# Kernel tuning notes

Measured on AMD Instinct MI355X. Metric: run time of the kernel, lower is better.

Reference implementation:

```python
import jax, jax.numpy as jnp
import numpy as np

LRELU = 0.2
EPS_LN = 1e-5
EPS_BN = 1e-5


def _seg_softmax(logits, seg, n):
    # softmax over edges grouped by destination node (PyG softmax), logits [E,H]
    m = jax.ops.segment_max(logits, seg, num_segments=n)
    e = jnp.exp(logits - m[seg])
    s = jax.ops.segment_sum(e, seg, num_segments=n)
    return e / (s[seg] + 1e-16)


def _gat(x, src, dst, n, W, a_src, a_dst, b, H, C):
    # PyG GATConv, concat=False (mean over heads), leaky_relu slope 0.2
    h = (x @ W).reshape(n, H, C)
    e = (h * a_src).sum(-1)[src] + (h * a_dst).sum(-1)[dst]  # [E,H]
    e = jnp.where(e > 0, e, LRELU * e)
    alpha = _seg_softmax(e, dst, n)
    out = jax.ops.segment_sum(h[src] * alpha[:, :, None], dst, num_segments=n)  # [N,H,C]
    return out.mean(1) + b


def _gcn(x, src, dst, n, W, b):
    # PyG GCNConv with symmetric normalization; edge list already contains self loops
    deg = jax.ops.segment_sum(jnp.ones(src.shape, x.dtype), dst, num_segments=n)
    dis = jnp.where(deg > 0, jax.lax.rsqrt(jnp.maximum(deg, 1e-12)), 0.0)
    h = x @ W
    w = (dis[src] * dis[dst])[:, None]
    return jax.ops.segment_sum(h[src] * w, dst, num_segments=n) + b


def _ln(x, g, b):
    mu = x.mean(-1, keepdims=True)
    v = x.var(-1, keepdims=True)
    return (x - mu) * jax.lax.rsqrt(v + EPS_LN) * g + b


def _bn_eval(x, g, b, rm, rv):
    return (x - rm) * jax.lax.rsqrt(rv + EPS_BN) * g + b


def _forward(x, edge_index, gin, bti, rmi, rvi, W1, as1, ad1, b1, Wg1, bg1,
             W2, as2, ad2, b2, Wg2, bg2, Ws, bs, Wf, bf,
             g1, be1, g2, be2, g3, be3, Wc1, bc1, gbn, bbn, rmb, rvb, Wc2, bc2):
    n = x.shape[0]
    xn = _bn_eval(x, gin, bti, rmi, rvi)
    sl = jnp.arange(n, dtype=edge_index.dtype)
    src = jnp.concatenate([edge_index[0], sl])
    dst = jnp.concatenate([edge_index[1], sl])
    # GAT1 (4 heads, 128) -> LN -> relu
    x1 = _gat(xn, src, dst, n, W1, as1, ad1, b1, 4, 128)
    x1 = jax.nn.relu(_ln(x1, g1, be1))
    # GCN1 -> relu
    x1g = jax.nn.relu(_gcn(x1, src, dst, n, Wg1, bg1))
    # GAT2 (2 heads, 64) -> LN -> relu
    x2 = _gat(x1g, src, dst, n, W2, as2, ad2, b2, 2, 64)
    x2 = jax.nn.relu(_ln(x2, g2, be2))
    # GCN2 -> relu
    x2g = jax.nn.relu(_gcn(x2, src, dst, n, Wg2, bg2))
    # skip + fusion
    skip = jax.nn.relu(xn @ Ws + bs)
    fused = jax.nn.relu(jnp.concatenate([x1g, x2g], axis=1) @ Wf + bf)
    final = _ln(fused + skip, g3, be3)
    # classifier: Linear -> BN(eval) -> relu -> Linear
    h = jax.nn.relu(_bn_eval(final @ Wc1 + bc1, gbn, bbn, rmb, rvb))
    return h @ Wc2 + bc2


def setup_inputs():
    key = jax.random.key(0)
    ks = jax.random.split(key, 20)
    N, F, E = 20000, 512, 160000
    H1, C1, H2, C2 = 4, 128, 2, 64
    rn = lambda k, sh, s=0.05: (jax.random.normal(k, sh) * s).astype(jnp.float32)
    return dict(
        x=jax.random.normal(ks[0], (N, F), jnp.float32),
        edge_index=jax.random.randint(ks[1], (2, E), 0, N, jnp.int32),
        gin=jnp.ones((F,), jnp.float32), bti=jnp.zeros((F,), jnp.float32),
        rmi=rn(ks[2], (F,)), rvi=(jax.random.uniform(ks[3], (F,)) + 0.5).astype(jnp.float32),
        W1=rn(ks[4], (F, H1 * C1)), as1=rn(ks[5], (H1, C1)), ad1=rn(ks[6], (H1, C1)), b1=jnp.zeros((C1,), jnp.float32),
        Wg1=rn(ks[7], (C1, C1)), bg1=jnp.zeros((C1,), jnp.float32),
        W2=rn(ks[8], (C1, H2 * C2)), as2=rn(ks[9], (H2, C2)), ad2=rn(ks[10], (H2, C2)), b2=jnp.zeros((C2,), jnp.float32),
        Wg2=rn(ks[11], (C2, C2)), bg2=jnp.zeros((C2,), jnp.float32),
        Ws=rn(ks[12], (F, C2)), bs=jnp.zeros((C2,), jnp.float32),
        Wf=rn(ks[13], (C1 + C2, C2)), bf=jnp.zeros((C2,), jnp.float32),
        g1=jnp.ones((C1,), jnp.float32), be1=jnp.zeros((C1,), jnp.float32),
        g2=jnp.ones((C2,), jnp.float32), be2=jnp.zeros((C2,), jnp.float32),
        g3=jnp.ones((C2,), jnp.float32), be3=jnp.zeros((C2,), jnp.float32),
        Wc1=rn(ks[14], (C2, 32)), bc1=jnp.zeros((32,), jnp.float32),
        gbn=jnp.ones((32,), jnp.float32), bbn=jnp.zeros((32,), jnp.float32),
        rmb=rn(ks[15], (32,)), rvb=(jax.random.uniform(ks[16], (32,)) + 0.5).astype(jnp.float32),
        Wc2=rn(ks[17], (32, 5)), bc2=jnp.zeros((5,), jnp.float32),
    )


def reference(x, edge_index, gin, bti, rmi, rvi, W1, as1, ad1, b1, Wg1, bg1,
              W2, as2, ad2, b2, Wg2, bg2, Ws, bs, Wf, bf,
              g1, be1, g2, be2, g3, be3, Wc1, bc1, gbn, bbn, rmb, rvb, Wc2, bc2):
    return _forward(x, edge_index, gin, bti, rmi, rvi, W1, as1, ad1, b1, Wg1, bg1,
                    W2, as2, ad2, b2, Wg2, bg2, Ws, bs, Wf, bf,
                    g1, be1, g2, be2, g3, be3, Wc1, bc1, gbn, bbn, rmb, rvb, Wc2, bc2)
```

## Files before the change

kernel.cpp:

```cpp
#include <hip/hip_runtime.h>
#include <hip/hip_bf16.h>

#define N_NODES 20000
#define F_IN 512

typedef __attribute__((ext_vector_type(8))) short short8;
typedef __attribute__((ext_vector_type(4))) float f32x4;

__device__ __forceinline__ ushort f2bf(float f) {
    uint u = __float_as_uint(f);
    u += 0x7FFF + ((u >> 16) & 1);
    return (ushort)(u >> 16);
}
__device__ __forceinline__ float bf2f(ushort h) { return __uint_as_float((uint)h << 16); }

__device__ __forceinline__ void gload_lds16(const void* g, void* l) {
    __builtin_amdgcn_global_load_lds(
        (const __attribute__((address_space(1))) void*)g,
        (__attribute__((address_space(3))) void*)l, 16, 0, 0);
}

__global__ void zero_int_k(int* p, int n) {
    int i = blockIdx.x * blockDim.x + threadIdx.x;
    if (i < n) p[i] = 0;
}

__global__ void hist_k(const int* __restrict__ ei, int E0, int N, int* __restrict__ deg) {
    int e = blockIdx.x * blockDim.x + threadIdx.x;
    int Etot = E0 + N;
    if (e >= Etot) return;
    int dst = (e < E0) ? ei[E0 + e] : (e - E0);
    atomicAdd(&deg[dst], 1);
}

__global__ __launch_bounds__(1024) void scan_k(const int* __restrict__ deg, int* __restrict__ rp,
                                               int* __restrict__ fp, float* __restrict__ dis,
                                               int N, int Etot) {
    __shared__ int part[1024];
    int tid = threadIdx.x;
    int chunk = (N + 1023) / 1024;
    int lo = tid * chunk, hi = min(lo + chunk, N);
    int s = 0;
    for (int i = lo; i < hi; i++) s += deg[i];
    part[tid] = s;
    __syncthreads();
    for (int off = 1; off < 1024; off <<= 1) {
        int t = 0;
        if (tid >= off) t = part[tid - off];
        __syncthreads();
        part[tid] += t;
        __syncthreads();
    }
    int run = part[tid] - s;
    for (int i = lo; i < hi; i++) {
        rp[i] = run; fp[i] = run;
        int d = deg[i];
        dis[i] = (d > 0) ? rsqrtf((float)d) : 0.f;
        run += d;
    }
    if (tid == 1023) { rp[N] = Etot; fp[N] = Etot; }
}

__global__ void scatter_k(const int* __restrict__ ei, int E0, int N, int* __restrict__ fp,
                          int* __restrict__ csr_src) {
    int e = blockIdx.x * blockDim.x + threadIdx.x;
    int Etot = E0 + N;
    if (e >= Etot) return;
    int src, dst;
    if (e < E0) { src = ei[e]; dst = ei[E0 + e]; }
    else        { src = e - E0; dst = src; }
    int pos = atomicAdd(&fp[dst], 1);
    csr_src[pos] = src;
}

__global__ void bnprep_k(const float* __restrict__ g, const float* __restrict__ b,
                         const float* __restrict__ rm, const float* __restrict__ rv,
                         float* __restrict__ sc, float* __restrict__ sh, int n) {
    int i = blockIdx.x * blockDim.x + threadIdx.x;
    if (i >= n) return;
    float s = g[i] * rsqrtf(rv[i] + 1e-5f);
    sc[i] = s;
    sh[i] = b[i] - rm[i] * s;
}

__global__ void splitA_k(const float* __restrict__ x, const float* __restrict__ sc,
                         const float* __restrict__ sh, ushort* __restrict__ Ah,
                         ushort* __restrict__ Al, int M, int Mpad) {
    size_t i4 = (size_t)blockIdx.x * blockDim.x + threadIdx.x;
    size_t base = i4 * 4;
    if (base >= (size_t)Mpad * 512) return;
    int row = (int)(base >> 9);
    ushort4 ah = {0, 0, 0, 0}, al = {0, 0, 0, 0};
    if (row < M) {
        float4 v = *(const float4*)&x[base];
        int c = (int)(base & 511);
        float f0 = v.x * sc[c] + sh[c];
        float f1 = v.y * sc[c + 1] + sh[c + 1];
        float f2 = v.z * sc[c + 2] + sh[c + 2];
        float f3 = v.w * sc[c + 3] + sh[c + 3];
        ah.x = f2bf(f0); al.x = f2bf(f0 - bf2f(ah.x));
        ah.y = f2bf(f1); al.y = f2bf(f1 - bf2f(ah.y));
        ah.z = f2bf(f2); al.z = f2bf(f2 - bf2f(ah.z));
        ah.w = f2bf(f3); al.w = f2bf(f3 - bf2f(ah.w));
    }
    *(ushort4*)&Ah[base] = ah;
    *(ushort4*)&Al[base] = al;
}

__global__ __launch_bounds__(256) void splitBt_k(const float* __restrict__ W1, const float* __restrict__ Ws,
                                                 ushort* __restrict__ Bth, ushort* __restrict__ Btl) {
    __shared__ float tile[64][65];
    int n0 = blockIdx.x * 64;
    int k0 = blockIdx.y * 64;
    int t = threadIdx.x;
    int a = t >> 6, b = t & 63;
#pragma unroll
    for (int i = 0; i < 16; i++) {
        int kk = a + i * 4, nn = b;
        int gk = k0 + kk, gn = n0 + nn;
        float v;
        if (gn < 512)      v = W1[(size_t)gk * 512 + gn];
        else if (gn < 576) v = Ws[(size_t)gk * 64 + (gn - 512)];
        else               v = 0.f;
        tile[kk][nn] = v;
    }
    __syncthreads();
#pragma unroll
    for (int i = 0; i < 16; i++) {
        int nn = a + i * 4, kk = b;
        float v = tile[kk][nn];
        ushort hi = f2bf(v);
        ushort lo = f2bf(v - bf2f(hi));
        Bth[(size_t)(n0 + nn) * 512 + k0 + kk] = hi;
        Btl[(size_t)(n0 + nn) * 512 + k0 + kk] = lo;
    }
}

__global__ __launch_bounds__(256) void mfma_gemm_k(
    const ushort* __restrict__ Ah, const ushort* __restrict__ Al,
    const ushort* __restrict__ Bth, const ushort* __restrict__ Btl,
    const float* __restrict__ bs, const float* __restrict__ as1, const float* __restrict__ ad1,
    float* __restrict__ h1, float* __restrict__ skip,
    float* __restrict__ ss1, float* __restrict__ sd1,
    int M, int K) {
    __shared__ ushort A_s[128 * 64];
    __shared__ ushort B_s[128 * 64];
    __shared__ float s1buf[128], s2buf[128];
    int t = threadIdx.x;
    int w = t >> 6, l = t & 63;

    int nwg = gridDim.x;
    int q = nwg >> 3, r = nwg & 7;
    int xcd = blockIdx.x & 7, lid = blockIdx.x >> 3;
    int wg = (xcd < r) ? xcd * (q + 1) + lid : r * (q + 1) + (xcd - r) * q + lid;
    int by = wg / 5, bx = wg % 5;
    int bm = by * 128;
    int n0 = bx * 128;
    int r0 = (w & 1) * 64, c0 = (w >> 1) * 64;

    f32x4 acc[4][4] = {};

    int sl = (t & 7) ^ ((t >> 3) & 7);
    const ushort* aArr = (sl < 4) ? Ah : Al;
    const ushort* bArr = (sl < 4) ? Bth : Btl;
    int ko = (sl & 3) * 8;
    size_t asrc[4], bsrc[4];
#pragma unroll
    for (int c = 0; c < 4; c++) {
        int rr = c * 32 + (t >> 3);
        asrc[c] = (size_t)(bm + rr) * 512 + ko;
        bsrc[c] = (size_t)(n0 + rr) * 512 + ko;
    }
    int d0 = t * 8;

    for (int kt = 0; kt < K; kt += 32) {
#pragma unroll
        for (int c = 0; c < 4; c++) gload_lds16(aArr + asrc[c] + kt, &A_s[c * 2048 + d0]);
#pragma unroll
        for (int c = 0; c < 4; c++) gload_lds16(bArr + bsrc[c] + kt, &B_s[c * 2048 + d0]);
        __syncthreads();

        short8 ah[4], al4[4], bh[4], bl[4];
        int lr = l & 15, kg = l >> 4;
        int spa = kg ^ (lr & 7);
#pragma unroll
        for (int f = 0; f < 4; f++) {
            int ra = (r0 + f * 16 + lr) * 64;
            ah[f]  = *(const short8*)&A_s[ra + spa * 8];
            al4[f] = *(const short8*)&A_s[ra + (spa ^ 4) * 8];
            int rb = (c0 + f * 16 + lr) * 64;
            bh[f] = *(const short8*)&B_s[rb + spa * 8];
            bl[f] = *(const short8*)&B_s[rb + (spa ^ 4) * 8];
        }
#pragma unroll
        for (int fm = 0; fm < 4; fm++)
#pragma unroll
            for (int fn = 0; fn < 4; fn++) {
                acc[fm][fn] = __builtin_amdgcn_mfma_f32_16x16x32_bf16(ah[fm], bh[fn], acc[fm][fn], 0, 0, 0);
                acc[fm][fn] = __builtin_amdgcn_mfma_f32_16x16x32_bf16(ah[fm], bl[fn], acc[fm][fn], 0, 0, 0);
                acc[fm][fn] = __builtin_amdgcn_mfma_f32_16x16x32_bf16(al4[fm], bh[fn], acc[fm][fn], 0, 0, 0);
            }
        __syncthreads();
    }

    int lr = l & 15, kg = l >> 4;
#pragma unroll
    for (int fm = 0; fm < 4; fm++) {
        int row_base = bm + r0 + fm * 16 + kg * 4;
#pragma unroll
        for (int fn = 0; fn < 4; fn++) {
            int col = n0 + c0 + fn * 16 + lr;
#pragma unroll
            for (int r2 = 0; r2 < 4; r2++) {
                int row = row_base + r2;
                if (row < M) {
                    float v = acc[fm][fn][r2];
                    if (col < 512) h1[(size_t)row * 512 + col] = v;
                    else if (col < 576) skip[(size_t)row * 64 + (col - 512)] = fmaxf(v + bs[col - 512], 0.f);
                }
            }
        }
    }

    if (t < 128) { s1buf[t] = 0.f; s2buf[t] = 0.f; }
    __syncthreads();
    if (bx < 4) {
        float aw_[4], dw_[4];
#pragma unroll
        for (int fn = 0; fn < 4; fn++) {
            int col = n0 + c0 + fn * 16 + lr;
            aw_[fn] = as1[col];
            dw_[fn] = ad1[col];
        }
#pragma unroll
        for (int fm = 0; fm < 4; fm++)
#pragma unroll
            for (int r2 = 0; r2 < 4; r2++) {
                float p1 = acc[fm][0][r2] * aw_[0] + acc[fm][1][r2] * aw_[1] +
                           acc[fm][2][r2] * aw_[2] + acc[fm][3][r2] * aw_[3];
                float p2 = acc[fm][0][r2] * dw_[0] + acc[fm][1][r2] * dw_[1] +
                           acc[fm][2][r2] * dw_[2] + acc[fm][3][r2] * dw_[3];
#pragma unroll
                for (int off = 1; off < 16; off <<= 1) {
                    p1 += __shfl_xor(p1, off);
                    p2 += __shfl_xor(p2, off);
                }
                if (lr == 0) {
                    int rloc = r0 + fm * 16 + kg * 4 + r2;
                    atomicAdd(&s1buf[rloc], p1);
                    atomicAdd(&s2buf[rloc], p2);
                }
            }
    }
    __syncthreads();
    if (bx < 4 && t < 128 && bm + t < M) {
        ss1[(size_t)(bm + t) * 4 + bx] = s1buf[t];
        sd1[(size_t)(bm + t) * 4 + bx] = s2buf[t];
    }
}

template <int K, int NOUT>
__global__ __launch_bounds__(NOUT) void rowgemm_k(const float* __restrict__ X, const float* __restrict__ W,
                                                  float* __restrict__ out, int N) {
    __shared__ float Ws[K * NOUT];
    __shared__ float Xs[8][K];
    int c = threadIdx.x;
    for (int i = c; i < K * NOUT; i += NOUT) Ws[i] = W[i];
    for (int r0 = blockIdx.x * 8; r0 < N; r0 += gridDim.x * 8) {
        int nr = min(8, N - r0);
        __syncthreads();
        for (int i = c; i < nr * K; i += NOUT) Xs[i / K][i % K] = X[(size_t)r0 * K + i];
        __syncthreads();
        float acc[8] = {};
        for (int k = 0; k < K; k++) {
            float w = Ws[k * NOUT + c];
#pragma unroll
            for (int r = 0; r < 8; r++) acc[r] += Xs[r][k] * w;
        }
        for (int r = 0; r < nr; r++) out[(size_t)(r0 + r) * NOUT + c] = acc[r];
    }
}

template <int H, int C>
__global__ __launch_bounds__(256) void scores_k(const float* __restrict__ h, const float* __restrict__ a_src,
                                                const float* __restrict__ a_dst, float* __restrict__ ss,
                                                float* __restrict__ sd, int N) {
    int wid = (blockIdx.x * blockDim.x + threadIdx.x) >> 6;
    int lane = threadIdx.x & 63;
    if (wid >= N * H) return;
    int hh = wid % H;
    const float* hp = h + (size_t)(wid / H) * (H * C) + hh * C;
    float s1 = 0.f, s2 = 0.f;
    for (int c = lane; c < C; c += 64) {
        float v = hp[c];
        s1 += v * a_src[hh * C + c];
        s2 += v * a_dst[hh * C + c];
    }
#pragma unroll
    for (int off = 32; off; off >>= 1) {
        s1 += __shfl_down(s1, off);
        s2 += __shfl_down(s2, off);
    }
    if (lane == 0) { ss[wid] = s1; sd[wid] = s2; }
}

template <int H, int C>
__global__ __launch_bounds__(C) void gat_agg_k(const float* __restrict__ h, const float* __restrict__ ss,
                                               const float* __restrict__ sd, const float* __restrict__ bias,
                                               const float* __restrict__ g, const float* __restrict__ be,
                                               const int* __restrict__ rp, const int* __restrict__ csr_src,
                                               float* __restrict__ out, int N) {
    int n = blockIdx.x;
    int tid = threadIdx.x;
    __shared__ float m_s[H], s_s[H], red[4];
    __shared__ int srcs[64];
    __shared__ float aw[64 * H];
    int e0 = rp[n], deg = rp[n + 1] - e0;
    bool small = (deg <= 64);
    int hh = tid >> 5, l = tid & 31;

    if (small && tid < deg) srcs[tid] = csr_src[e0 + tid];
    __syncthreads();

    float sdv = sd[n * H + hh];
    float m = -1e30f, s = 0.f;
    for (int k = l; k < deg; k += 32) {
        int src = small ? srcs[k] : csr_src[e0 + k];
        float e = ss[src * H + hh] + sdv;
        e = (e > 0.f) ? e : 0.2f * e;
        if (small) aw[k * H + hh] = e;
        float mn = fmaxf(m, e);
        s = s * __expf(m - mn) + __expf(e - mn);
        m = mn;
    }
#pragma unroll
    for (int off = 16; off; off >>= 1) {
        float mo = __shfl_xor(m, off), so = __shfl_xor(s, off);
        float mn = fmaxf(m, mo);
        s = s * __expf(m - mn) + so * __expf(mo - mn);
        m = mn;
    }
    if (l == 0) { m_s[hh] = m; s_s[hh] = s + 1e-16f; }
    __syncthreads();

    float v = 0.f;
    if (small) {
        for (int idx = tid; idx < deg * H; idx += C) {
            int h2 = idx & (H - 1);
            aw[idx] = __expf(aw[idx] - m_s[h2]) / s_s[h2];
        }
        __syncthreads();
        for (int k = 0; k < deg; k++) {
            const float* hp = h + (size_t)srcs[k] * (H * C) + tid;
#pragma unroll
            for (int h2 = 0; h2 < H; h2++) v += aw[k * H + h2] * hp[h2 * C];
        }
    } else {
        for (int t0 = 0; t0 < deg; t0 += 64) {
            int tl = min(64, deg - t0);
            __syncthreads();
            if (tid < tl) srcs[tid] = csr_src[e0 + t0 + tid];
            __syncthreads();
            for (int idx = tid; idx < tl * H; idx += C) {
                int k = idx / H, h2 = idx & (H - 1);
                float e = ss[srcs[k] * H + h2] + sd[n * H + h2];
                e = (e > 0.f) ? e : 0.2f * e;
                aw[idx] = __expf(e - m_s[h2]) / s_s[h2];
            }
            __syncthreads();
            for (int k = 0; k < tl; k++) {
                const float* hp = h + (size_t)srcs[k] * (H * C) + tid;
#pragma unroll
                for (int h2 = 0; h2 < H; h2++) v += aw[k * H + h2] * hp[h2 * C];
            }
        }
    }

    v = v * (1.f / H) + bias[tid];
    float t1 = v;
#pragma unroll
    for (int off = 32; off; off >>= 1) t1 += __shfl_xor(t1, off);
    float mu;
    if (C == 128) {
        if ((tid & 63) == 0) red[tid >> 6] = t1;
        __syncthreads();
        mu = (red[0] + red[1]) * (1.f / C);
    } else {
        mu = t1 * (1.f / C);
    }
    float d = v - mu;
    float t2 = d * d;
#pragma unroll
    for (int off = 32; off; off >>= 1) t2 += __shfl_xor(t2, off);
    float var;
    if (C == 128) {
        if ((tid & 63) == 0) red[2 + (tid >> 6)] = t2;
        __syncthreads();
        var = (red[2] + red[3]) * (1.f / C);
    } else {
        var = t2 * (1.f / C);
    }
    float y = d * rsqrtf(var + 1e-5f) * g[tid] + be[tid];
    out[(size_t)n * C + tid] = fmaxf(y, 0.f);
}

template <int C>
__global__ __launch_bounds__(C) void gcn_agg_k(const float* __restrict__ h, const float* __restrict__ dis,
                                               const float* __restrict__ bias, const int* __restrict__ rp,
                                               const int* __restrict__ csr_src, float* __restrict__ out, int N) {
    int n = blockIdx.x;
    int tid = threadIdx.x;
    __shared__ int srcs[64];
    __shared__ float w[64];
    int e0 = rp[n], deg = rp[n + 1] - e0;
    float dn = dis[n];
    float acc = 0.f;
    for (int t0 = 0; t0 < deg; t0 += 64) {
        int tl = min(64, deg - t0);
        if (tid < tl) {
            int s = csr_src[e0 + t0 + tid];
            srcs[tid] = s;
            w[tid] = dis[s] * dn;
        }
        __syncthreads();
        for (int k = 0; k < tl; k++) acc += w[k] * h[(size_t)srcs[k] * C + tid];
        __syncthreads();
    }
    out[(size_t)n * C + tid] = fmaxf(acc + bias[tid], 0.f);
}

__global__ __launch_bounds__(64) void final_fused_k(
    const float* __restrict__ hg2, const float* __restrict__ dis, const float* __restrict__ bg2,
    const int* __restrict__ rp, const int* __restrict__ csr_src,
    const float* __restrict__ x1g, const float* __restrict__ Wf, const float* __restrict__ bf,
    const float* __restrict__ skip, const float* __restrict__ g3, const float* __restrict__ be3,
    const float* __restrict__ Wc1, const float* __restrict__ bc1, const float* __restrict__ gbn,
    const float* __restrict__ bbn, const float* __restrict__ rmb, const float* __restrict__ rvb,
    const float* __restrict__ Wc2, const float* __restrict__ bc2, float* __restrict__ out, int N) {
    int n = blockIdx.x;
    int tid = threadIdx.x;
    __shared__ int srcs[64];
    __shared__ float w[64];
    __shared__ float cat[192];
    __shared__ float fbuf[64];
    __shared__ float hbuf[32];
    int e0 = rp[n], deg = rp[n + 1] - e0;
    float dn = dis[n];
    float acc = 0.f;
    for (int t0 = 0; t0 < deg; t0 += 64) {
        int tl = min(64, deg - t0);
        if (tid < tl) {
            int s = csr_src[e0 + t0 + tid];
            srcs[tid] = s;
            w[tid] = dis[s] * dn;
        }
        __syncthreads();
        for (int k = 0; k < tl; k++) acc += w[k] * hg2[(size_t)srcs[k] * 64 + tid];
        __syncthreads();
    }
    float x2gv = fmaxf(acc + bg2[tid], 0.f);
    cat[tid] = x1g[(size_t)n * 128 + tid];
    cat[64 + tid] = x1g[(size_t)n * 128 + 64 + tid];
    cat[128 + tid] = x2gv;
    __syncthreads();
    float fa = bf[tid];
    for (int j = 0; j < 192; j++) fa += cat[j] * Wf[j * 64 + tid];
    fa = fmaxf(fa, 0.f) + skip[(size_t)n * 64 + tid];
    float t1 = fa;
#pragma unroll
    for (int off = 32; off; off >>= 1) t1 += __shfl_xor(t1, off);
    float mu = t1 * (1.f / 64.f);
    float d = fa - mu;
    float t2 = d * d;
#pragma unroll
    for (int off = 32; off; off >>= 1) t2 += __shfl_xor(t2, off);
    float var = t2 * (1.f / 64.f);
    fbuf[tid] = d * rsqrtf(var + 1e-5f) * g3[tid] + be3[tid];
    __syncthreads();
    if (tid < 32) {
        float a = bc1[tid];
        for (int j = 0; j < 64; j++) a += fbuf[j] * Wc1[j * 32 + tid];
        a = (a - rmb[tid]) * rsqrtf(rvb[tid] + 1e-5f) * gbn[tid] + bbn[tid];
        hbuf[tid] = fmaxf(a, 0.f);
    }
    __syncthreads();
    if (tid < 5) {
        float a = bc2[tid];
        for (int j = 0; j < 32; j++) a += hbuf[j] * Wc2[j * 5 + tid];
        out[(size_t)n * 5 + tid] = a;
    }
}

extern "C" void kernel_launch(void* const* d_in, const int* in_sizes, int n_in,
                              void* d_out, int out_size, void* d_ws, size_t ws_size,
                              hipStream_t stream) {
    const float* x   = (const float*)d_in[0];
    const int*   ei  = (const int*)d_in[1];
    const float* gin = (const float*)d_in[2];
    const float* bti = (const float*)d_in[3];
    const float* rmi = (const float*)d_in[4];
    const float* rvi = (const float*)d_in[5];
    const float* W1  = (const float*)d_in[6];
    const float* as1 = (const float*)d_in[7];
    const float* ad1 = (const float*)d_in[8];
    const float* b1  = (const float*)d_in[9];
    const float* Wg1 = (const float*)d_in[10];
    const float* bg1 = (const float*)d_in[11];
    const float* W2  = (const float*)d_in[12];
    const float* as2 = (const float*)d_in[13];
    const float* ad2 = (const float*)d_in[14];
    const float* b2  = (const float*)d_in[15];
    const float* Wg2 = (const float*)d_in[16];
    const float* bg2 = (const float*)d_in[17];
    const float* Ws  = (const float*)d_in[18];
    const float* bs  = (const float*)d_in[19];
    const float* Wf  = (const float*)d_in[20];
    const float* bf  = (const float*)d_in[21];
    const float* g1  = (const float*)d_in[22];
    const float* be1 = (const float*)d_in[23];
    const float* g2  = (const float*)d_in[24];
    const float* be2 = (const float*)d_in[25];
    const float* g3  = (const float*)d_in[26];
    const float* be3 = (const float*)d_in[27];
    const float* Wc1 = (const float*)d_in[28];
    const float* bc1 = (const float*)d_in[29];
    const float* gbn = (const float*)d_in[30];
    const float* bbn = (const float*)d_in[31];
    const float* rmb = (const float*)d_in[32];
    const float* rvb = (const float*)d_in[33];
    const float* Wc2 = (const float*)d_in[34];
    const float* bc2 = (const float*)d_in[35];
    float* out = (float*)d_out;

    const int N = in_sizes[0] / F_IN;
    const int E0 = in_sizes[1] / 2;
    const int Etot = E0 + N;
    const int Mpad = 20096;

    char* wp = (char*)d_ws;
    auto alloc = [&](size_t bytes) -> void* {
        void* p = (void*)wp;
        wp += (bytes + 255) & ~(size_t)255;
        return p;
    };
    float* h1   = (float*)alloc((size_t)N * 512 * 4);
    ushort* Ah  = (ushort*)alloc((size_t)Mpad * 512 * 2);
    ushort* Al  = (ushort*)alloc((size_t)Mpad * 512 * 2);
    ushort* Bth = (ushort*)alloc((size_t)640 * 512 * 2);
    ushort* Btl = (ushort*)alloc((size_t)640 * 512 * 2);
    float* skip = (float*)alloc((size_t)N * 64 * 4);
    float* ss1  = (float*)alloc((size_t)N * 4 * 4);
    float* sd1  = (float*)alloc((size_t)N * 4 * 4);
    float* ss2  = (float*)alloc((size_t)N * 2 * 4);
    float* sd2  = (float*)alloc((size_t)N * 2 * 4);
    float* dis  = (float*)alloc((size_t)N * 4);
    float* sc   = (float*)alloc((size_t)F_IN * 4);
    float* sh   = (float*)alloc((size_t)F_IN * 4);
    int* deg    = (int*)alloc((size_t)N * 4);
    int* rp     = (int*)alloc((size_t)(N + 1) * 4);
    int* fp     = (int*)alloc((size_t)(N + 1) * 4);
    int* csr    = (int*)alloc((size_t)Etot * 4);
    float* hg1 = h1;
    float* x1g = h1 + (size_t)N * 128;
    float* h2  = h1 + (size_t)N * 256;
    float* x2  = h1 + (size_t)N * 384;
    float* hg2 = h1 + (size_t)N * 448;
    float* x1  = (float*)Ah;

    zero_int_k<<<(N + 255) / 256, 256, 0, stream>>>(deg, N);
    hist_k<<<(Etot + 255) / 256, 256, 0, stream>>>(ei, E0, N, deg);
    scan_k<<<1, 1024, 0, stream>>>(deg, rp, fp, dis, N, Etot);
    scatter_k<<<(Etot + 255) / 256, 256, 0, stream>>>(ei, E0, N, fp, csr);
    bnprep_k<<<2, 256, 0, stream>>>(gin, bti, rmi, rvi, sc, sh, F_IN);
    splitA_k<<<(int)(((size_t)Mpad * 512 / 4 + 255) / 256), 256, 0, stream>>>(x, sc, sh, Ah, Al, N, Mpad);
    splitBt_k<<<dim3(10, 8), 256, 0, stream>>>(W1, Ws, Bth, Btl);

    mfma_gemm_k<<<785, 256, 0, stream>>>(Ah, Al, Bth, Btl, bs, as1, ad1, h1, skip, ss1, sd1, N, 512);

    gat_agg_k<4, 128><<<N, 128, 0, stream>>>(h1, ss1, sd1, b1, g1, be1, rp, csr, x1, N);

    rowgemm_k<128, 128><<<1280, 128, 0, stream>>>(x1, Wg1, hg1, N);
    gcn_agg_k<128><<<N, 128, 0, stream>>>(hg1, dis, bg1, rp, csr, x1g, N);

    rowgemm_k<128, 128><<<1280, 128, 0, stream>>>(x1g, W2, h2, N);
    scores_k<2, 64><<<(N * 2 + 3) / 4, 256, 0, stream>>>(h2, as2, ad2, ss2, sd2, N);
    gat_agg_k<2, 64><<<N, 64, 0, stream>>>(h2, ss2, sd2, b2, g2, be2, rp, csr, x2, N);

    rowgemm_k<64, 64><<<1280, 64, 0, stream>>>(x2, Wg2, hg2, N);

    final_fused_k<<<N, 64, 0, stream>>>(hg2, dis, bg2, rp, csr, x1g, Wf, bf, skip, g3, be3,
                                        Wc1, bc1, gbn, bbn, rmb, rvb, Wc2, bc2, out, N);
}
```

Measured before the change: 540.5 us.

## Vectorize edge-gather aggregation, fuse GAT2 scores into GEMM, pack final kernel per wave

GAT and GCN aggregation kernels now have each thread load float4 chunks and process several edges in parallel per block, then reduce partial sums across lanes and through shared memory. The GAT2 attention-score computation moves into the epilogue of the preceding row GEMM, which removes the separate scores kernel and its re-read of h2. The final fused kernel handles four nodes per 256-thread block, one wavefront per node, with no block barriers. The aim is wider memory transactions and fewer launches and syncs, at the cost of more shuffle reductions and extra per-row shuffle work inside the GEMM.

```diff
diff --git a/kernel.cpp b/kernel.cpp
--- a/kernel.cpp
+++ b/kernel.cpp
@@ -18,6 +18,13 @@
     __builtin_amdgcn_global_load_lds(
         (const __attribute__((address_space(1))) void*)g,
         (__attribute__((address_space(3))) void*)l, 16, 0, 0);
+}
+
+__device__ __forceinline__ f32x4 shfl_xor4(f32x4 v, int m) {
+    f32x4 r;
+#pragma unroll
+    for (int i = 0; i < 4; i++) r[i] = __shfl_xor(v[i], m);
+    return r;
 }
 
 __global__ void zero_int_k(int* p, int n) {
@@ -259,13 +266,17 @@
     }
 }
 
-template <int K, int NOUT>
+template <int K, int NOUT, bool SC>
 __global__ __launch_bounds__(NOUT) void rowgemm_k(const float* __restrict__ X, const float* __restrict__ W,
-                                                  float* __restrict__ out, int N) {
+                                                  float* __restrict__ out,
+                                                  const float* __restrict__ a_src, const float* __restrict__ a_dst,
+                                                  float* __restrict__ ss, float* __restrict__ sd, int N) {
     __shared__ float Ws[K * NOUT];
     __shared__ float Xs[8][K];
     int c = threadIdx.x;
     for (int i = c; i < K * NOUT; i += NOUT) Ws[i] = W[i];
+    float asv = 0.f, adv = 0.f;
+    if (SC) { asv = a_src[c]; adv = a_dst[c]; }
     for (int r0 = blockIdx.x * 8; r0 < N; r0 += gridDim.x * 8) {
         int nr = min(8, N - r0);
         __syncthreads();
@@ -278,30 +289,22 @@
             for (int r = 0; r < 8; r++) acc[r] += Xs[r][k] * w;
         }
         for (int r = 0; r < nr; r++) out[(size_t)(r0 + r) * NOUT + c] = acc[r];
-    }
-}
-
-template <int H, int C>
-__global__ __launch_bounds__(256) void scores_k(const float* __restrict__ h, const float* __restrict__ a_src,
-                                                const float* __restrict__ a_dst, float* __restrict__ ss,
-                                                float* __restrict__ sd, int N) {
-    int wid = (blockIdx.x * blockDim.x + threadIdx.x) >> 6;
-    int lane = threadIdx.x & 63;
-    if (wid >= N * H) return;
-    int hh = wid % H;
-    const float* hp = h + (size_t)(wid / H) * (H * C) + hh * C;
-    float s1 = 0.f, s2 = 0.f;
-    for (int c = lane; c < C; c += 64) {
-        float v = hp[c];
-        s1 += v * a_src[hh * C + c];
-        s2 += v * a_dst[hh * C + c];
-    }
-#pragma unroll
-    for (int off = 32; off; off >>= 1) {
-        s1 += __shfl_down(s1, off);
-        s2 += __shfl_down(s2, off);
-    }
-    if (lane == 0) { ss[wid] = s1; sd[wid] = s2; }
+        if (SC) {
+            int head = c >> 6;
+            for (int r = 0; r < nr; r++) {
+                float p1 = acc[r] * asv, p2 = acc[r] * adv;
+#pragma unroll
+                for (int off = 1; off < 64; off <<= 1) {
+                    p1 += __shfl_xor(p1, off);
+                    p2 += __shfl_xor(p2, off);
+                }
+                if ((c & 63) == 0) {
+                    ss[(size_t)(r0 + r) * 2 + head] = p1;
+                    sd[(size_t)(r0 + r) * 2 + head] = p2;
+                }
+            }
+        }
+    }
 }
 
 template <int H, int C>
@@ -312,7 +315,8 @@
                                                float* __restrict__ out, int N) {
     int n = blockIdx.x;
     int tid = threadIdx.x;
-    __shared__ float m_s[H], s_s[H], red[4];
+    __shared__ float m_s[H], s_s[H];
+    __shared__ __align__(16) float red4[32][4];
     __shared__ int srcs[64];
     __shared__ float aw[64 * H];
     int e0 = rp[n], deg = rp[n + 1] - e0;
@@ -343,17 +347,25 @@
     if (l == 0) { m_s[hh] = m; s_s[hh] = s + 1e-16f; }
     __syncthreads();
 
-    float v = 0.f;
+    constexpr int LPR = H * C / 4;
+    constexpr int EIF = C / LPR;
+    int ep = tid / LPR;
+    int o  = (tid % LPR) * 4;
+    int hq = o / C;
+    f32x4 acc = {0.f, 0.f, 0.f, 0.f};
+
     if (small) {
         for (int idx = tid; idx < deg * H; idx += C) {
             int h2 = idx & (H - 1);
             aw[idx] = __expf(aw[idx] - m_s[h2]) / s_s[h2];
         }
         __syncthreads();
-        for (int k = 0; k < deg; k++) {
-            const float* hp = h + (size_t)srcs[k] * (H * C) + tid;
-#pragma unroll
-            for (int h2 = 0; h2 < H; h2++) v += aw[k * H + h2] * hp[h2 * C];
+        for (int k = 0; k < deg; k += EIF) {
+            int e = k + ep;
+            if (EIF == 1 || e < deg) {
+                f32x4 v = *(const f32x4*)(h + (size_t)srcs[e] * (H * C) + o);
+                acc += aw[e * H + hq] * v;
+            }
         }
     } else {
         for (int t0 = 0; t0 < deg; t0 += 64) {
@@ -368,53 +380,79 @@
                 aw[idx] = __expf(e - m_s[h2]) / s_s[h2];
             }
             __syncthreads();
-            for (int k = 0; k < tl; k++) {
-                const float* hp = h + (size_t)srcs[k] * (H * C) + tid;
-#pragma unroll
-                for (int h2 = 0; h2 < H; h2++) v += aw[k * H + h2] * hp[h2 * C];
-            }
-        }
-    }
-
-    v = v * (1.f / H) + bias[tid];
-    float t1 = v;
-#pragma unroll
-    for (int off = 32; off; off >>= 1) t1 += __shfl_xor(t1, off);
-    float mu;
-    if (C == 128) {
-        if ((tid & 63) == 0) red[tid >> 6] = t1;
-        __syncthreads();
-        mu = (red[0] + red[1]) * (1.f / C);
+            for (int k = 0; k < tl; k += EIF) {
+                int e = k + ep;
+                if (EIF == 1 || e < tl) {
+                    f32x4 v = *(const f32x4*)(h + (size_t)srcs[e] * (H * C) + o);
+                    acc += aw[e * H + hq] * v;
+                }
+            }
+        }
+    }
+
+    if (H == 4) {
+        acc += shfl_xor4(acc, 32);
+        if (tid >= 64 && (tid & 63) < 32) *(f32x4*)&red4[tid & 31][0] = acc;
+        __syncthreads();
+        if (tid < 32) {
+            f32x4 o2 = *(const f32x4*)&red4[tid][0];
+            acc += o2;
+            f32x4 b4 = *(const f32x4*)&bias[tid * 4];
+            f32x4 v4 = acc * 0.25f + b4;
+            float s1 = v4[0] + v4[1] + v4[2] + v4[3];
+#pragma unroll
+            for (int off = 1; off < 32; off <<= 1) s1 += __shfl_xor(s1, off);
+            float mu = s1 * (1.f / C);
+            f32x4 d4 = v4 - mu;
+            float s2 = d4[0]*d4[0] + d4[1]*d4[1] + d4[2]*d4[2] + d4[3]*d4[3];
+#pragma unroll
+            for (int off = 1; off < 32; off <<= 1) s2 += __shfl_xor(s2, off);
+            float rs = rsqrtf(s2 * (1.f / C) + 1e-5f);
+            f32x4 g4 = *(const f32x4*)&g[tid * 4];
+            f32x4 e4 = *(const f32x4*)&be[tid * 4];
+            f32x4 y;
+#pragma unroll
+            for (int i = 0; i < 4; i++) y[i] = fmaxf(d4[i] * rs * g4[i] + e4[i], 0.f);
+            *(f32x4*)(out + (size_t)n * C + tid * 4) = y;
+        }
     } else {
-        mu = t1 * (1.f / C);
-    }
-    float d = v - mu;
-    float t2 = d * d;
-#pragma unroll
-    for (int off = 32; off; off >>= 1) t2 += __shfl_xor(t2, off);
-    float var;
-    if (C == 128) {
-        if ((tid & 63) == 0) red[2 + (tid >> 6)] = t2;
-        __syncthreads();
-        var = (red[2] + red[3]) * (1.f / C);
-    } else {
-        var = t2 * (1.f / C);
-    }
-    float y = d * rsqrtf(var + 1e-5f) * g[tid] + be[tid];
-    out[(size_t)n * C + tid] = fmaxf(y, 0.f);
-}
-
-template <int C>
-__global__ __launch_bounds__(C) void gcn_agg_k(const float* __restrict__ h, const float* __restrict__ dis,
-                                               const float* __restrict__ bias, const int* __restrict__ rp,
-                                               const int* __restrict__ csr_src, float* __restrict__ out, int N) {
+        acc += shfl_xor4(acc, 32);
+        acc += shfl_xor4(acc, 16);
+        if (tid < 16) {
+            f32x4 b4 = *(const f32x4*)&bias[tid * 4];
+            f32x4 v4 = acc * 0.5f + b4;
+            float s1 = v4[0] + v4[1] + v4[2] + v4[3];
+#pragma unroll
+            for (int off = 1; off < 16; off <<= 1) s1 += __shfl_xor(s1, off);
+            float mu = s1 * (1.f / C);
+            f32x4 d4 = v4 - mu;
+            float s2 = d4[0]*d4[0] + d4[1]*d4[1] + d4[2]*d4[2] + d4[3]*d4[3];
+#pragma unroll
+            for (int off = 1; off < 16; off <<= 1) s2 += __shfl_xor(s2, off);
+            float rs = rsqrtf(s2 * (1.f / C) + 1e-5f);
+            f32x4 g4 = *(const f32x4*)&g[tid * 4];
+            f32x4 e4 = *(const f32x4*)&be[tid * 4];
+            f32x4 y;
+#pragma unroll
+            for (int i = 0; i < 4; i++) y[i] = fmaxf(d4[i] * rs * g4[i] + e4[i], 0.f);
+            *(f32x4*)(out + (size_t)n * C + tid * 4) = y;
+        }
+    }
+}
+
+__global__ __launch_bounds__(128) void gcn_agg128_k(const float* __restrict__ h, const float* __restrict__ dis,
+                                                    const float* __restrict__ bias, const int* __restrict__ rp,
+                                                    const int* __restrict__ csr_src, float* __restrict__ out, int N) {
     int n = blockIdx.x;
     int tid = threadIdx.x;
     __shared__ int srcs[64];
     __shared__ float w[64];
+    __shared__ __align__(16) float red4[32][4];
     int e0 = rp[n], deg = rp[n + 1] - e0;
     float dn = dis[n];
-    float acc = 0.f;
+    int ep = tid >> 5;
+    int c0 = (tid & 31) * 4;
+    f32x4 acc = {0.f, 0.f, 0.f, 0.f};
     for (int t0 = 0; t0 < deg; t0 += 64) {
         int tl = min(64, deg - t0);
         if (tid < tl) {
@@ -423,13 +461,30 @@
             w[tid] = dis[s] * dn;
         }
         __syncthreads();
-        for (int k = 0; k < tl; k++) acc += w[k] * h[(size_t)srcs[k] * C + tid];
-        __syncthreads();
-    }
-    out[(size_t)n * C + tid] = fmaxf(acc + bias[tid], 0.f);
-}
-
-__global__ __launch_bounds__(64) void final_fused_k(
+        for (int k = 0; k < tl; k += 4) {
+            int e = k + ep;
+            if (e < tl) {
+                f32x4 v = *(const f32x4*)(h + (size_t)srcs[e] * 128 + c0);
+                acc += w[e] * v;
+            }
+        }
+        __syncthreads();
+    }
+    acc += shfl_xor4(acc, 32);
+    if (tid >= 64 && (tid & 63) < 32) *(f32x4*)&red4[tid & 31][0] = acc;
+    __syncthreads();
+    if (tid < 32) {
+        f32x4 o2 = *(const f32x4*)&red4[tid][0];
+        acc += o2;
+        f32x4 b4 = *(const f32x4*)&bias[c0];
+        f32x4 y;
+#pragma unroll
+        for (int i = 0; i < 4; i++) y[i] = fmaxf(acc[i] + b4[i], 0.f);
+        *(f32x4*)(out + (size_t)n * 128 + c0) = y;
+    }
+}
+
+__global__ __launch_bounds__(256) void final_fused_k(
     const float* __restrict__ hg2, const float* __restrict__ dis, const float* __restrict__ bg2,
     const int* __restrict__ rp, const int* __restrict__ csr_src,
     const float* __restrict__ x1g, const float* __restrict__ Wf, const float* __restrict__ bf,
@@ -437,57 +492,61 @@
     const float* __restrict__ Wc1, const float* __restrict__ bc1, const float* __restrict__ gbn,
     const float* __restrict__ bbn, const float* __restrict__ rmb, const float* __restrict__ rvb,
     const float* __restrict__ Wc2, const float* __restrict__ bc2, float* __restrict__ out, int N) {
-    int n = blockIdx.x;
-    int tid = threadIdx.x;
-    __shared__ int srcs[64];
-    __shared__ float w[64];
-    __shared__ float cat[192];
-    __shared__ float fbuf[64];
-    __shared__ float hbuf[32];
+    int wv = threadIdx.x >> 6;
+    int t  = threadIdx.x & 63;
+    int n = blockIdx.x * 4 + wv;
+    __shared__ __align__(16) float cat_s[4][192];
+    __shared__ float fbuf_s[4][64];
+    __shared__ float hbuf_s[4][32];
+    if (n >= N) return;
+
     int e0 = rp[n], deg = rp[n + 1] - e0;
     float dn = dis[n];
-    float acc = 0.f;
-    for (int t0 = 0; t0 < deg; t0 += 64) {
-        int tl = min(64, deg - t0);
-        if (tid < tl) {
-            int s = csr_src[e0 + t0 + tid];
-            srcs[tid] = s;
-            w[tid] = dis[s] * dn;
-        }
-        __syncthreads();
-        for (int k = 0; k < tl; k++) acc += w[k] * hg2[(size_t)srcs[k] * 64 + tid];
-        __syncthreads();
-    }
-    float x2gv = fmaxf(acc + bg2[tid], 0.f);
-    cat[tid] = x1g[(size_t)n * 128 + tid];
-    cat[64 + tid] = x1g[(size_t)n * 128 + 64 + tid];
-    cat[128 + tid] = x2gv;
-    __syncthreads();
-    float fa = bf[tid];
-    for (int j = 0; j < 192; j++) fa += cat[j] * Wf[j * 64 + tid];
-    fa = fmaxf(fa, 0.f) + skip[(size_t)n * 64 + tid];
+    int ep = t >> 4;
+    int o = (t & 15) * 4;
+    f32x4 acc = {0.f, 0.f, 0.f, 0.f};
+    for (int k = 0; k < deg; k += 4) {
+        int e = k + ep;
+        if (e < deg) {
+            int s = csr_src[e0 + e];
+            f32x4 v = *(const f32x4*)(hg2 + (size_t)s * 64 + o);
+            acc += (dis[s] * dn) * v;
+        }
+    }
+    acc += shfl_xor4(acc, 32);
+    acc += shfl_xor4(acc, 16);
+    if (t < 16) {
+        f32x4 b4 = *(const f32x4*)&bg2[t * 4];
+        f32x4 xv;
+#pragma unroll
+        for (int i = 0; i < 4; i++) xv[i] = fmaxf(acc[i] + b4[i], 0.f);
+        *(f32x4*)&cat_s[wv][128 + t * 4] = xv;
+    }
+    if (t < 32) *(f32x4*)&cat_s[wv][t * 4] = *(const f32x4*)(x1g + (size_t)n * 128 + t * 4);
+    float fa = bf[t];
+    const float* cat = cat_s[wv];
+    for (int j = 0; j < 192; j++) fa += cat[j] * Wf[j * 64 + t];
+    fa = fmaxf(fa, 0.f) + skip[(size_t)n * 64 + t];
     float t1 = fa;
 #pragma unroll
-    for (int off = 32; off; off >>= 1) t1 += __shfl_xor(t1, off);
+    for (int off = 1; off < 64; off <<= 1) t1 += __shfl_xor(t1, off);
     float mu = t1 * (1.f / 64.f);
     float d = fa - mu;
     float t2 = d * d;
 #pragma unroll
-    for (int off = 32; off; off >>= 1) t2 += __shfl_xor(t2, off);
+    for (int off = 1; off < 64; off <<= 1) t2 += __shfl_xor(t2, off);
     float var = t2 * (1.f / 64.f);
-    fbuf[tid] = d * rsqrtf(var + 1e-5f) * g3[tid] + be3[tid];
-    __syncthreads();
-    if (tid < 32) {
-        float a = bc1[tid];
-        for (int j = 0; j < 64; j++) a += fbuf[j] * Wc1[j * 32 + tid];
-        a = (a - rmb[tid]) * rsqrtf(rvb[tid] + 1e-5f) * gbn[tid] + bbn[tid];
-        hbuf[tid] = fmaxf(a, 0.f);
-    }
-    __syncthreads();
-    if (tid < 5) {
-        float a = bc2[tid];
-        for (int j = 0; j < 32; j++) a += hbuf[j] * Wc2[j * 5 + tid];
-        out[(size_t)n * 5 + tid] = a;
+    fbuf_s[wv][t] = d * rsqrtf(var + 1e-5f) * g3[t] + be3[t];
+    if (t < 32) {
+        float a = bc1[t];
+        for (int j = 0; j < 64; j++) a += fbuf_s[wv][j] * Wc1[j * 32 + t];
+        a = (a - rmb[t]) * rsqrtf(rvb[t] + 1e-5f) * gbn[t] + bbn[t];
+        hbuf_s[wv][t] = fmaxf(a, 0.f);
+    }
+    if (t < 5) {
+        float a = bc2[t];
+        for (int j = 0; j < 32; j++) a += hbuf_s[wv][j] * Wc2[j * 5 + t];
+        out[(size_t)n * 5 + t] = a;
     }
 }
 
@@ -579,15 +638,14 @@
 
     gat_agg_k<4, 128><<<N, 128, 0, stream>>>(h1, ss1, sd1, b1, g1, be1, rp, csr, x1, N);
 
-    rowgemm_k<128, 128><<<1280, 128, 0, stream>>>(x1, Wg1, hg1, N);
-    gcn_agg_k<128><<<N, 128, 0, stream>>>(hg1, dis, bg1, rp, csr, x1g, N);
-
-    rowgemm_k<128, 128><<<1280, 128, 0, stream>>>(x1g, W2, h2, N);
-    scores_k<2, 64><<<(N * 2 + 3) / 4, 256, 0, stream>>>(h2, as2, ad2, ss2, sd2, N);
+    rowgemm_k<128, 128, false><<<1280, 128, 0, stream>>>(x1, Wg1, hg1, nullptr, nullptr, nullptr, nullptr, N);
+    gcn_agg128_k<<<N, 128, 0, stream>>>(hg1, dis, bg1, rp, csr, x1g, N);
+
+    rowgemm_k<128, 128, true><<<1280, 128, 0, stream>>>(x1g, W2, h2, as2, ad2, ss2, sd2, N);
     gat_agg_k<2, 64><<<N, 64, 0, stream>>>(h2, ss2, sd2, b2, g2, be2, rp, csr, x2, N);
 
-    rowgemm_k<64, 64><<<1280, 64, 0, stream>>>(x2, Wg2, hg2, N);
-
-    final_fused_k<<<N, 64, 0, stream>>>(hg2, dis, bg2, rp, csr, x1g, Wf, bf, skip, g3, be3,
-                                        Wc1, bc1, gbn, bbn, rmb, rvb, Wc2, bc2, out, N);
-}
+    rowgemm_k<64, 64, false><<<1280, 64, 0, stream>>>(x2, Wg2, hg2, nullptr, nullptr, nullptr, nullptr, N);
+
+    final_fused_k<<<(N + 3) / 4, 256, 0, stream>>>(hg2, dis, bg2, rp, csr, x1g, Wf, bf, skip, g3, be3,
+                                                   Wc1, bc1, gbn, bbn, rmb, rvb, Wc2, bc2, out, N);
+}
```

Result: slower. 555.5 us (+2.8%).
